# Performance work log

Hardware: AMD Instinct MI355X
Metric: run time of the kernel (lower is better)

Reference implementation:

```python
import jax, jax.numpy as jnp
import numpy as np

EMBED_DIM = 584  # module-global, used as softmax scale base (C ** -0.5)


def setup_inputs() -> dict:
    key = jax.random.key(0)
    ks = jax.random.split(key, 7)
    B, T, C, H, D = 16, 1024, 584, 8, 73
    x = jax.random.normal(ks[0], (B, T, C), dtype=jnp.float32)
    memory = jax.random.normal(ks[1], (B, T, C), dtype=jnp.float32)
    s = 0.02
    Wq = jax.random.normal(ks[2], (H, C, D), dtype=jnp.float32) * s
    Wk = jax.random.normal(ks[3], (H, C, D), dtype=jnp.float32) * s
    Wv = jax.random.normal(ks[4], (H, C, D), dtype=jnp.float32) * s
    Wp = jax.random.normal(ks[5], (C, C), dtype=jnp.float32) * s
    bp = jnp.zeros((C,), dtype=jnp.float32)
    return {"x": x, "memory": memory, "Wq": Wq, "Wk": Wk, "Wv": Wv, "Wp": Wp, "bp": bp}


def reference(x, memory, Wq, Wk, Wv, Wp, bp):
    B, T, C = x.shape
    # per-head projections, vectorized over heads: [B, H, T, D]
    q = jnp.einsum('btc,hcd->bhtd', x, Wq)
    k = jnp.einsum('bsc,hcd->bhsd', memory, Wk)
    v = jnp.einsum('btc,hcd->bhtd', x, Wv)  # NOTE: value from x, per original code
    # scale uses full embed dim C (not head size), per original code
    scores = jnp.einsum('bhtd,bhsd->bhts', q, k) * (C ** -0.5)
    weights = jax.nn.softmax(scores, axis=-1)
    # dropout is identity in eval/reference mode
    out = jnp.einsum('bhts,bhsd->bhtd', weights, v)  # requires S == T (matches original)
    out = out.transpose(0, 2, 1, 3).reshape(B, T, C)  # concat heads on last dim
    out = out @ Wp + bp  # output projection (dropout identity)
    return out
```

## Files before the change

### kernel.cpp

```cpp
#include <hip/hip_runtime.h>
#include <hip/hip_bf16.h>

typedef unsigned short u16;
typedef __attribute__((ext_vector_type(4))) unsigned short u16x4;
typedef __attribute__((ext_vector_type(8))) unsigned short u16x8;
typedef __attribute__((ext_vector_type(8))) __bf16 bf16x8;
typedef __attribute__((ext_vector_type(4))) float f32x4;

#define BB 16
#define TSEQ 1024
#define CC 584
#define HH 8
#define DHD 73
#define NR (BB*TSEQ)
#define KPW 640
#define DP 96
#define HD (HH*DP)
#define NP3 768
#define PPITCH 88
#define CEXP 0.0596985934f

__device__ __forceinline__ u16 f2bf(float f) {
  __bf16 h = (__bf16)f;
  return __builtin_bit_cast(u16, h);
}
__device__ __forceinline__ bf16x8 as_bf(u16x8 v) { return __builtin_bit_cast(bf16x8, v); }

#define GLL16(g, l) __builtin_amdgcn_global_load_lds( \
    (const __attribute__((address_space(1))) void*)(g), \
    (__attribute__((address_space(3))) void*)(l), 16, 0, 0)

#define BARRIER() asm volatile("s_barrier" ::: "memory")
#define LGKM0()   asm volatile("s_waitcnt lgkmcnt(0)" ::: "memory")
#define VMW4()    asm volatile("s_waitcnt vmcnt(4)" ::: "memory")
#define VMW0()    asm volatile("s_waitcnt vmcnt(0)" ::: "memory")

#define PKA 10240
#define PKB 5760
#define PKC 1920
__global__ void pack_all_kernel(const float* __restrict__ x, const float* __restrict__ mem,
                                const float* __restrict__ Wq, const float* __restrict__ Wk,
                                const float* __restrict__ Wv, const float* __restrict__ Wp,
                                u16* __restrict__ xmb, u16* __restrict__ wt,
                                u16* __restrict__ wpt) {
  const int bidx = blockIdx.x;
  const int tid = threadIdx.x;
  if (bidx < PKA) {
    int idx = bidx * 256 + tid;
    int row = idx / (KPW / 8);
    int c8  = (idx % (KPW / 8)) * 8;
    u16x8 o = {0, 0, 0, 0, 0, 0, 0, 0};
    if (c8 < CC) {
      const float* src = (row < NR) ? &x[(size_t)row * CC + c8]
                                    : &mem[(size_t)(row - NR) * CC + c8];
      f32x4 a = *(const f32x4*)src;
      f32x4 b = *(const f32x4*)(src + 4);
#pragma unroll
      for (int t = 0; t < 4; t++) { o[t] = f2bf(a[t]); o[4 + t] = f2bf(b[t]); }
    }
    *(u16x8*)&xmb[(size_t)row * KPW + c8] = o;
  } else if (bidx < PKA + PKB) {
    int idx = (bidx - PKA) * 256 + tid;
    int w   = idx / (HD * KPW);
    int rem = idx % (HD * KPW);
    int n = rem / KPW;
    int k = rem % KPW;
    int h = n / DP, d = n % DP;
    u16 val = 0;
    if (d < DHD && k < CC) {
      const float* W = (w == 0) ? Wq : ((w == 1) ? Wv : Wk);
      val = f2bf(W[((size_t)h * CC + k) * DHD + d]);
    }
    wt[idx] = val;
  } else {
    int idx = (bidx - PKA - PKB) * 256 + tid;
    int n = idx / KPW;
    int c = idx % KPW;
    u16 val = 0;
    if (n < CC && c < CC) val = f2bf(Wp[(size_t)c * CC + n]);
    wpt[idx] = val;
  }
}


template <int B, int MH>
__device__ __forceinline__ void lda_f(bf16x8 (&av)[4][2], const u16* lds,
                                      int aRow, int sw0, int sw1) {
#pragma unroll
  for (int mq = 0; mq < 4; mq++) {
    const int r = aRow + B * 16384 + MH * 4096 + mq * 1024;
    av[mq][0] = as_bf(*(const u16x8*)&lds[r + sw0]);
    av[mq][1] = as_bf(*(const u16x8*)&lds[r + sw1]);
  }
}
template <int B, int NH>
__device__ __forceinline__ void ldb_f(bf16x8 (&bv)[2][2], const u16* lds,
                                      int bRow, int sw0, int sw1) {
#pragma unroll
  for (int nq = 0; nq < 2; nq++) {
    const int r = 32768 + bRow + B * 16384 + NH * 2048 + nq * 1024;
    bv[nq][0] = as_bf(*(const u16x8*)&lds[r + sw0]);
    bv[nq][1] = as_bf(*(const u16x8*)&lds[r + sw1]);
  }
}
template <int OP, int U>
__device__ __forceinline__ void stg_f(const u16* g0, u16* l0, int t) {
  GLL16(g0 + (size_t)(U * 64) * KPW + (size_t)t * 64,
        l0 + OP * 32768 + (t & 1) * 16384 + U * 4096);
}
template <int MH, int NH>
__device__ __forceinline__ void mm_f(f32x4 (&acc)[8][4], const bf16x8 (&av)[4][2],
                                     const bf16x8 (&bv)[2][2]) {
  __builtin_amdgcn_s_setprio(1);
#pragma unroll
  for (int mq = 0; mq < 4; mq++)
#pragma unroll
    for (int nq = 0; nq < 2; nq++) {
      f32x4 c = acc[MH * 4 + mq][NH * 2 + nq];
      c = __builtin_amdgcn_mfma_f32_16x16x32_bf16(av[mq][0], bv[nq][0], c, 0, 0, 0);
      c = __builtin_amdgcn_mfma_f32_16x16x32_bf16(av[mq][1], bv[nq][1], c, 0, 0, 0);
      acc[MH * 4 + mq][NH * 2 + nq] = c;
    }
  __builtin_amdgcn_s_setprio(0);
}

template <int MODE>
__global__ __launch_bounds__(512, 2) void gemm8_kernel(
    const u16* __restrict__ A, const u16* __restrict__ Bt,
    void* __restrict__ CoutV, void* __restrict__ CoutV2,
    const float* __restrict__ bias) {
  extern __shared__ u16 lds[];
  const int tid  = threadIdx.x;
  const int lane = tid & 63;
  const int q15  = lane & 15;
  const int quad = lane >> 4;
  const int wave = tid >> 6;
  const int wmi  = wave >> 2;
  const int wni  = wave & 3;

  const int cpx = gridDim.x >> 3;
  const int bid = (blockIdx.x & 7) * cpx + (blockIdx.x >> 3);

  int m0, n0, npart;
  if (MODE == 4) {
    if (bid < 384) {
      m0 = (bid / 6) * 256; int nt = bid % 6;
      n0 = nt * 256; npart = (nt >= 3) ? 1 : 0;
    } else {
      int b2 = bid - 384;
      m0 = NR + (b2 / 3) * 256; n0 = 1536 + (b2 % 3) * 256; npart = 2;
    }
  } else {
    m0 = (bid / 3) * 256; n0 = (bid % 3) * 256; npart = 0;
  }

  const int tr   = tid >> 3;
  const int scol = ((tid & 7) ^ (tr & 7)) * 8;
  const u16* gA = &A[(size_t)(m0 + tr) * KPW + scol];
  const u16* gB = &Bt[(size_t)(n0 + tr) * KPW + scol];
  u16* ldst = &lds[tid * 8];

  const int rb  = q15 & 7;
  const int sw0 = (quad ^ rb) * 8;
  const int sw1 = ((quad + 4) ^ rb) * 8;
  const int aRow = (wmi * 128 + q15) * 64;
  const int bRow = (wni * 64 + q15) * 64;

  f32x4 acc[8][4];
#pragma unroll
  for (int i = 0; i < 8; i++)
#pragma unroll
    for (int j = 0; j < 4; j++) acc[i][j] = (f32x4){0.f, 0.f, 0.f, 0.f};
  bf16x8 av[4][2], bv[2][2];

  stg_f<0,0>(gA, ldst, 0); stg_f<0,1>(gA, ldst, 0);
  stg_f<0,2>(gA, ldst, 0); stg_f<0,3>(gA, ldst, 0);
  stg_f<1,0>(gB, ldst, 0); stg_f<1,1>(gB, ldst, 0);
  stg_f<1,2>(gB, ldst, 0); stg_f<1,3>(gB, ldst, 0);
  stg_f<0,0>(gA, ldst, 1); stg_f<0,2>(gA, ldst, 1);
  stg_f<0,1>(gA, ldst, 1); stg_f<0,3>(gA, ldst, 1);
  VMW4(); BARRIER();

#pragma unroll 1
  for (int i = 0; i < 5; ++i) {
    const int t1 = 2 * i + 1;
    const int t2 = 2 * i + 2;
    const bool st = (i < 4);
    lda_f<0,0>(av, lds, aRow, sw0, sw1);
    ldb_f<0,0>(bv, lds, bRow, sw0, sw1);
    stg_f<1,0>(gB, ldst, t1); stg_f<1,1>(gB, ldst, t1);
    stg_f<1,2>(gB, ldst, t1); stg_f<1,3>(gB, ldst, t1);
    BARRIER(); LGKM0();
    mm_f<0,0>(acc, av, bv);
    BARRIER();
    ldb_f<0,1>(bv, lds, bRow, sw0, sw1);
    if (st) { stg_f<0,0>(gA, ldst, t2); stg_f<0,2>(gA, ldst, t2); }
    BARRIER(); LGKM0();
    mm_f<0,1>(acc, av, bv);
    BARRIER();
    lda_f<0,1>(av, lds, aRow, sw0, sw1);
    ldb_f<0,0>(bv, lds, bRow, sw0, sw1);
    BARRIER(); LGKM0();
    mm_f<1,0>(acc, av, bv);
    BARRIER();
    ldb_f<0,1>(bv, lds, bRow, sw0, sw1);
    if (st) { stg_f<0,1>(gA, ldst, t2); stg_f<0,3>(gA, ldst, t2); }
    BARRIER(); LGKM0();
    mm_f<1,1>(acc, av, bv);
    if (st) { VMW4(); } else { VMW0(); }
    BARRIER();
    lda_f<1,0>(av, lds, aRow, sw0, sw1);
    ldb_f<1,0>(bv, lds, bRow, sw0, sw1);
    if (st) { stg_f<1,0>(gB, ldst, t2); stg_f<1,1>(gB, ldst, t2); }
    BARRIER(); LGKM0();
    mm_f<0,0>(acc, av, bv);
    BARRIER();
    ldb_f<1,1>(bv, lds, bRow, sw0, sw1);
    if (st) { stg_f<1,2>(gB, ldst, t2); stg_f<1,3>(gB, ldst, t2); }
    BARRIER(); LGKM0();
    mm_f<0,1>(acc, av, bv);
    BARRIER();
    lda_f<1,1>(av, lds, aRow, sw0, sw1);
    ldb_f<1,0>(bv, lds, bRow, sw0, sw1);
    if (st) { stg_f<0,0>(gA, ldst, t1 + 2); stg_f<0,2>(gA, ldst, t1 + 2); }
    BARRIER(); LGKM0();
    mm_f<1,0>(acc, av, bv);
    BARRIER();
    ldb_f<1,1>(bv, lds, bRow, sw0, sw1);
    if (st) { stg_f<0,1>(gA, ldst, t1 + 2); stg_f<0,3>(gA, ldst, t1 + 2); }
    BARRIER(); LGKM0();
    mm_f<1,1>(acc, av, bv);
    if (st) { VMW4(); }
    BARRIER();
  }

  const int rowb = m0 + wmi * 128 + quad * 4;
  const int colb = n0 + wni * 64 + q15;
  if (MODE == 4) {
    if (npart == 2) {
      u16* Cout = (u16*)CoutV2;
#pragma unroll
      for (int mf = 0; mf < 8; mf++)
#pragma unroll
        for (int nf = 0; nf < 4; nf++) {
          const int rk = rowb + mf * 16 - NR;
          const int ck = colb + nf * 16 - 1536;
#pragma unroll
          for (int r = 0; r < 4; r++)
            Cout[(size_t)(rk + r) * HD + ck] = f2bf(acc[mf][nf][r]);
        }
    } else if (npart == 0) {
      u16* Cout = (u16*)CoutV;
#pragma unroll
      for (int mf = 0; mf < 8; mf++)
#pragma unroll
        for (int nf = 0; nf < 4; nf++) {
          const int row = rowb + mf * 16;
          const int col = colb + nf * 16;
#pragma unroll
          for (int r = 0; r < 4; r++)
            Cout[(size_t)(row + r) * HD + col] = f2bf(acc[mf][nf][r]);
        }
    } else {
      u16* Cout = (u16*)CoutV;
#pragma unroll
      for (int mf = 0; mf < 8; mf++) {
        const int row = rowb + mf * 16;
        const int bb  = row >> 10;
        const int tl  = row & 1023;
#pragma unroll
        for (int nf = 0; nf < 4; nf++) {
          const int vn = colb + nf * 16 - HD;
          u16x4 pk;
#pragma unroll
          for (int r = 0; r < 4; r++) pk[r] = f2bf(acc[mf][nf][r]);
          *(u16x4*)&Cout[(size_t)(NR * HD) + ((size_t)(bb * HD + vn)) * TSEQ + tl] = pk;
        }
      }
    }
  } else {
    float* Cout = (float*)CoutV;
#pragma unroll
    for (int mf = 0; mf < 8; mf++)
#pragma unroll
      for (int nf = 0; nf < 4; nf++) {
        const int col = colb + nf * 16;
        if (col < CC) {
          const float bvv = bias[col];
          const int row = rowb + mf * 16;
#pragma unroll
          for (int r = 0; r < 4; r++)
            Cout[(size_t)(row + r) * CC + col] = acc[mf][nf][r] + bvv;
        }
      }
  }
}

__global__ __launch_bounds__(256, 3) void attn_kernel(
    const u16* __restrict__ qb, const u16* __restrict__ kb,
    const u16* __restrict__ vt, u16* __restrict__ attn) {
  __shared__ u16 smem[128 * 96 + 64 * 104 + 96 * 72];
  u16* Qs = smem;
  u16* Ks = smem + 128 * 96;
  u16* Vs = smem + 128 * 96 + 64 * 104;
  u16* Pt = smem;

  const int tid  = threadIdx.x;
  const int lane = tid & 63;
  const int wave = tid >> 6;
  const int q15  = lane & 15;
  const int quad = lane >> 4;
  const int bid  = blockIdx.x;
  const int loc  = bid >> 3;
  const int pair = (bid & 7) * 16 + (loc >> 3);
  const int b  = pair >> 3;
  const int h  = pair & 7;
  const int t0 = (loc & 7) * 128;
  const int wq0 = wave * 32;

  int krow[3], kc[3], vrow[3], vc[3];
#pragma unroll
  for (int p = 0; p < 3; p++) {
    int qk = tid + 256 * p;
    krow[p] = qk / 12; kc[p] = (qk % 12) * 8;
    int qv = tid + 256 * p;
    vrow[p] = qv / 8;  vc[p] = (qv % 8) * 8;
  }
  const u16* kbase = &kb[(size_t)(b * TSEQ) * HD + h * DP];
  const u16* vbase = &vt[(size_t)(b * HD + h * DP) * TSEQ];

  for (int q = tid; q < 128 * 12; q += 256) {
    int row = q / 12, c8 = (q % 12) * 8;
    *(u16x8*)&Qs[row * 96 + c8] =
        *(const u16x8*)&qb[(size_t)(b * TSEQ + t0 + row) * HD + h * DP + c8];
  }
  if (tid < 128) {
    const u16x8 z = {0, 0, 0, 0, 0, 0, 0, 0};
    size_t base = (size_t)(b * TSEQ + t0 + tid) * KPW + CC;
#pragma unroll
    for (int c = 0; c < (KPW - CC) / 8; c++) *(u16x8*)&attn[base + c * 8] = z;
  }
  __syncthreads();

  bf16x8 aq[2][3];
#pragma unroll
  for (int n = 0; n < 2; n++)
#pragma unroll
    for (int kcx = 0; kcx < 3; kcx++)
      aq[n][kcx] = as_bf(*(const u16x8*)&Qs[(wq0 + n * 16 + q15) * 96 + kcx * 32 + quad * 8]);

  float lsum[2] = {0.f, 0.f};
  f32x4 oacc[2][6];
#pragma unroll
  for (int m = 0; m < 2; m++)
#pragma unroll
    for (int jd = 0; jd < 6; jd++) oacc[m][jd] = (f32x4){0.f, 0.f, 0.f, 0.f};

  u16* Ptw = &Pt[wave * 32 * PPITCH];

  u16x8 kreg[3], vreg[3];
#pragma unroll
  for (int p = 0; p < 3; p++) {
    kreg[p] = *(const u16x8*)&kbase[(size_t)krow[p] * HD + kc[p]];
    vreg[p] = *(const u16x8*)&vbase[(size_t)vrow[p] * TSEQ + vc[p]];
  }

  for (int si = 0; si < 16; ++si) {
#pragma unroll
    for (int p = 0; p < 3; p++) {
      *(u16x8*)&Ks[krow[p] * 104 + kc[p]] = kreg[p];
      *(u16x8*)&Vs[vrow[p] * 72 + vc[p]]  = vreg[p];
    }
    __syncthreads();

    if (si < 15) {
      const int s1 = (si + 1) * 64;
#pragma unroll
      for (int p = 0; p < 3; p++) {
        kreg[p] = *(const u16x8*)&kbase[(size_t)(s1 + krow[p]) * HD + kc[p]];
        vreg[p] = *(const u16x8*)&vbase[(size_t)vrow[p] * TSEQ + s1 + vc[p]];
      }
    }

    f32x4 st[4][2];
#pragma unroll
    for (int mt = 0; mt < 4; mt++)
#pragma unroll
      for (int n = 0; n < 2; n++) st[mt][n] = (f32x4){0.f, 0.f, 0.f, 0.f};
#pragma unroll
    for (int kcx = 0; kcx < 3; kcx++) {
      bf16x8 ak[4];
#pragma unroll
      for (int mt = 0; mt < 4; mt++)
        ak[mt] = as_bf(*(const u16x8*)&Ks[(mt * 16 + q15) * 104 + kcx * 32 + quad * 8]);
#pragma unroll
      for (int mt = 0; mt < 4; mt++)
#pragma unroll
        for (int n = 0; n < 2; n++)
          st[mt][n] = __builtin_amdgcn_mfma_f32_16x16x32_bf16(ak[mt], aq[n][kcx], st[mt][n], 0, 0, 0);
    }

#pragma unroll
    for (int mt = 0; mt < 4; mt++)
#pragma unroll
      for (int n = 0; n < 2; n++) {
        f32x4 pv;
#pragma unroll
        for (int r = 0; r < 4; r++) pv[r] = __builtin_amdgcn_exp2f(st[mt][n][r] * CEXP);
        lsum[n] += (pv[0] + pv[1]) + (pv[2] + pv[3]);
        u16x4 pk;
#pragma unroll
        for (int r = 0; r < 4; r++) pk[r] = f2bf(pv[r]);
        *(u16x4*)&Ptw[(n * 16 + q15) * PPITCH + mt * 16 + quad * 4] = pk;
      }

#pragma unroll
    for (int kcx = 0; kcx < 2; kcx++) {
      bf16x8 ap[2];
#pragma unroll
      for (int m = 0; m < 2; m++)
        ap[m] = as_bf(*(const u16x8*)&Ptw[(m * 16 + q15) * PPITCH + kcx * 32 + quad * 8]);
#pragma unroll
      for (int jd = 0; jd < 6; jd++) {
        bf16x8 bv = as_bf(*(const u16x8*)&Vs[(jd * 16 + q15) * 72 + kcx * 32 + quad * 8]);
#pragma unroll
        for (int m = 0; m < 2; m++)
          oacc[m][jd] = __builtin_amdgcn_mfma_f32_16x16x32_bf16(ap[m], bv, oacc[m][jd], 0, 0, 0);
      }
    }
    __syncthreads();
  }

  float lr[2];
#pragma unroll
  for (int n = 0; n < 2; n++) {
    float s = lsum[n];
    s += __shfl_xor(s, 16);
    s += __shfl_xor(s, 32);
    lr[n] = s;
  }

#pragma unroll
  for (int m = 0; m < 2; m++) {
#pragma unroll
    for (int r = 0; r < 4; r++) {
      const float inv = 1.f / __shfl(lr[m], quad * 4 + r);
      const int trow = t0 + wq0 + m * 16 + quad * 4 + r;
#pragma unroll
      for (int jd = 0; jd < 5; jd++) {
        const int d = jd * 16 + q15;
        if (d < DHD)
          attn[(size_t)(b * TSEQ + trow) * KPW + h * DHD + d] = f2bf(oacc[m][jd][r] * inv);
      }
    }
  }
}


extern "C" void kernel_launch(void* const* d_in, const int* in_sizes, int n_in,
                              void* d_out, int out_size, void* d_ws, size_t ws_size,
                              hipStream_t stream) {
  const float* x   = (const float*)d_in[0];
  const float* mem = (const float*)d_in[1];
  const float* Wq  = (const float*)d_in[2];
  const float* Wk  = (const float*)d_in[3];
  const float* Wv  = (const float*)d_in[4];
  const float* Wp  = (const float*)d_in[5];
  const float* bp  = (const float*)d_in[6];
  float* out = (float*)d_out;

  char* ws = (char*)d_ws;
  const size_t SZ_XMB = (size_t)2 * NR * KPW * 2;
  const size_t SZ_WT  = (size_t)3 * HD * KPW * 2;
  const size_t SZ_WPT = (size_t)NP3 * KPW * 2;
  const size_t SZ_QB  = (size_t)NR * HD * 2;

  u16* xmb    = (u16*)(ws);
  u16* attn_o = (u16*)(ws);
  u16* wt     = (u16*)(ws + SZ_XMB);
  u16* wp_t   = (u16*)(ws + SZ_XMB + SZ_WT);
  u16* q_buf  = (u16*)(ws + SZ_XMB + SZ_WT + SZ_WPT);
  u16* vt_buf = q_buf + (size_t)NR * HD;
  u16* k_buf  = (u16*)(ws + SZ_XMB + SZ_WT + SZ_WPT + 2 * SZ_QB);

  (void)in_sizes; (void)n_in; (void)out_size; (void)ws_size;

  static bool s_attr = false;
  if (!s_attr) {
    (void)hipFuncSetAttribute((const void*)gemm8_kernel<4>,
                              hipFuncAttributeMaxDynamicSharedMemorySize, 131072);
    (void)hipFuncSetAttribute((const void*)gemm8_kernel<2>,
                              hipFuncAttributeMaxDynamicSharedMemorySize, 131072);
    s_attr = true;
  }

  pack_all_kernel<<<PKA + PKB + PKC, 256, 0, stream>>>(x, mem, Wq, Wk, Wv, Wp,
                                                       xmb, wt, wp_t);

  gemm8_kernel<4><<<576, 512, 131072, stream>>>(xmb, wt, q_buf, k_buf, nullptr);

  attn_kernel<<<BB * HH * (TSEQ / 128), 256, 0, stream>>>(q_buf, k_buf, vt_buf, attn_o);

  gemm8_kernel<2><<<192, 512, 131072, stream>>>(attn_o, wp_t, out, nullptr, bp);
}
```

Before: 292.2 us.

## Replace fine-grained 8-phase GEMM schedule with simple per-tile double-buffered loop

Replaces the hand-interleaved schedule, which had many barriers and half-tile LDS reads and global-to-LDS stages per iteration, with a plain loop. Each iteration loads the whole 64-wide K tile of A and B fragments from LDS, issues all MFMAs, then prefetches tile t+2 into the freed buffer, with two barriers per tile. This removes most barrier and lgkm wait overhead and lets the compiler schedule LDS reads against MFMAs. In exchange it uses more fragment registers and overlaps global loads with compute less finely.

```diff
diff --git a/kernel.cpp b/kernel.cpp
--- a/kernel.cpp
+++ b/kernel.cpp
@@ -14,6 +14,7 @@
 #define DHD 73
 #define NR (BB*TSEQ)
 #define KPW 640
+#define KT64 10
 #define DP 96
 #define HD (HH*DP)
 #define NP3 768
@@ -31,8 +32,7 @@
     (__attribute__((address_space(3))) void*)(l), 16, 0, 0)
 
 #define BARRIER() asm volatile("s_barrier" ::: "memory")
-#define LGKM0()   asm volatile("s_waitcnt lgkmcnt(0)" ::: "memory")
-#define VMW4()    asm volatile("s_waitcnt vmcnt(4)" ::: "memory")
+#define VMW8()    asm volatile("s_waitcnt vmcnt(8)" ::: "memory")
 #define VMW0()    asm volatile("s_waitcnt vmcnt(0)" ::: "memory")
 
 #define PKA 10240
@@ -83,31 +83,6 @@
 }
 
 
-template <int B, int MH>
-__device__ __forceinline__ void lda_f(bf16x8 (&av)[4][2], const u16* lds,
-                                      int aRow, int sw0, int sw1) {
-#pragma unroll
-  for (int mq = 0; mq < 4; mq++) {
-    const int r = aRow + B * 16384 + MH * 4096 + mq * 1024;
-    av[mq][0] = as_bf(*(const u16x8*)&lds[r + sw0]);
-    av[mq][1] = as_bf(*(const u16x8*)&lds[r + sw1]);
-  }
-}
-template <int B, int NH>
-__device__ __forceinline__ void ldb_f(bf16x8 (&bv)[2][2], const u16* lds,
-                                      int bRow, int sw0, int sw1) {
-#pragma unroll
-  for (int nq = 0; nq < 2; nq++) {
-    const int r = 32768 + bRow + B * 16384 + NH * 2048 + nq * 1024;
-    bv[nq][0] = as_bf(*(const u16x8*)&lds[r + sw0]);
-    bv[nq][1] = as_bf(*(const u16x8*)&lds[r + sw1]);
-  }
-}
-template <int OP, int U>
-__device__ __forceinline__ void stg_f(const u16* g0, u16* l0, int t) {
-  GLL16(g0 + (size_t)(U * 64) * KPW + (size_t)t * 64,
-        l0 + OP * 32768 + (t & 1) * 16384 + U * 4096);
-}
 template <int MH, int NH>
 __device__ __forceinline__ void mm_f(f32x4 (&acc)[8][4], const bf16x8 (&av)[4][2],
                                      const bf16x8 (&bv)[2][2]) {
@@ -122,6 +97,53 @@
       acc[MH * 4 + mq][NH * 2 + nq] = c;
     }
   __builtin_amdgcn_s_setprio(0);
+}
+
+__device__ __forceinline__ void compute_tile(f32x4 (&acc)[8][4], const u16* lds,
+                                             int bufA, int aRow, int bRow,
+                                             int sw0, int sw1) {
+  const int bufB = bufA + 32768;
+  bf16x8 a0[4][2], a1[4][2], b0[2][2], b1[2][2];
+#pragma unroll
+  for (int mq = 0; mq < 4; mq++) {
+    const int r = bufA + aRow + mq * 1024;
+    a0[mq][0] = as_bf(*(const u16x8*)&lds[r + sw0]);
+    a0[mq][1] = as_bf(*(const u16x8*)&lds[r + sw1]);
+  }
+#pragma unroll
+  for (int nq = 0; nq < 2; nq++) {
+    const int r = bufB + bRow + nq * 1024;
+    b0[nq][0] = as_bf(*(const u16x8*)&lds[r + sw0]);
+    b0[nq][1] = as_bf(*(const u16x8*)&lds[r + sw1]);
+  }
+#pragma unroll
+  for (int nq = 0; nq < 2; nq++) {
+    const int r = bufB + bRow + 2048 + nq * 1024;
+    b1[nq][0] = as_bf(*(const u16x8*)&lds[r + sw0]);
+    b1[nq][1] = as_bf(*(const u16x8*)&lds[r + sw1]);
+  }
+#pragma unroll
+  for (int mq = 0; mq < 4; mq++) {
+    const int r = bufA + aRow + 4096 + mq * 1024;
+    a1[mq][0] = as_bf(*(const u16x8*)&lds[r + sw0]);
+    a1[mq][1] = as_bf(*(const u16x8*)&lds[r + sw1]);
+  }
+  mm_f<0, 0>(acc, a0, b0);
+  mm_f<0, 1>(acc, a0, b1);
+  mm_f<1, 1>(acc, a1, b1);
+  mm_f<1, 0>(acc, a1, b0);
+}
+
+__device__ __forceinline__ void stage_all(const u16* gA, const u16* gB,
+                                          u16* ldst, int t) {
+  const size_t ko = (size_t)t * 64;
+  const int lb = (t & 1) * 16384;
+#pragma unroll
+  for (int U = 0; U < 4; U++)
+    GLL16(gA + (size_t)(U * 64) * KPW + ko, ldst + lb + U * 4096);
+#pragma unroll
+  for (int U = 0; U < 4; U++)
+    GLL16(gB + (size_t)(U * 64) * KPW + ko, ldst + 32768 + lb + U * 4096);
 }
 
 template <int MODE>
@@ -171,66 +193,22 @@
   for (int i = 0; i < 8; i++)
 #pragma unroll
     for (int j = 0; j < 4; j++) acc[i][j] = (f32x4){0.f, 0.f, 0.f, 0.f};
-  bf16x8 av[4][2], bv[2][2];
-
-  stg_f<0,0>(gA, ldst, 0); stg_f<0,1>(gA, ldst, 0);
-  stg_f<0,2>(gA, ldst, 0); stg_f<0,3>(gA, ldst, 0);
-  stg_f<1,0>(gB, ldst, 0); stg_f<1,1>(gB, ldst, 0);
-  stg_f<1,2>(gB, ldst, 0); stg_f<1,3>(gB, ldst, 0);
-  stg_f<0,0>(gA, ldst, 1); stg_f<0,2>(gA, ldst, 1);
-  stg_f<0,1>(gA, ldst, 1); stg_f<0,3>(gA, ldst, 1);
-  VMW4(); BARRIER();
+
+  stage_all(gA, gB, ldst, 0);
+  stage_all(gA, gB, ldst, 1);
+  VMW8(); BARRIER();
 
 #pragma unroll 1
-  for (int i = 0; i < 5; ++i) {
-    const int t1 = 2 * i + 1;
-    const int t2 = 2 * i + 2;
-    const bool st = (i < 4);
-    lda_f<0,0>(av, lds, aRow, sw0, sw1);
-    ldb_f<0,0>(bv, lds, bRow, sw0, sw1);
-    stg_f<1,0>(gB, ldst, t1); stg_f<1,1>(gB, ldst, t1);
-    stg_f<1,2>(gB, ldst, t1); stg_f<1,3>(gB, ldst, t1);
-    BARRIER(); LGKM0();
-    mm_f<0,0>(acc, av, bv);
+  for (int t = 0; t < KT64; ++t) {
+    compute_tile(acc, lds, (t & 1) * 16384, aRow, bRow, sw0, sw1);
+    if (t == KT64 - 1) break;
     BARRIER();
-    ldb_f<0,1>(bv, lds, bRow, sw0, sw1);
-    if (st) { stg_f<0,0>(gA, ldst, t2); stg_f<0,2>(gA, ldst, t2); }
-    BARRIER(); LGKM0();
-    mm_f<0,1>(acc, av, bv);
-    BARRIER();
-    lda_f<0,1>(av, lds, aRow, sw0, sw1);
-    ldb_f<0,0>(bv, lds, bRow, sw0, sw1);
-    BARRIER(); LGKM0();
-    mm_f<1,0>(acc, av, bv);
-    BARRIER();
-    ldb_f<0,1>(bv, lds, bRow, sw0, sw1);
-    if (st) { stg_f<0,1>(gA, ldst, t2); stg_f<0,3>(gA, ldst, t2); }
-    BARRIER(); LGKM0();
-    mm_f<1,1>(acc, av, bv);
-    if (st) { VMW4(); } else { VMW0(); }
-    BARRIER();
-    lda_f<1,0>(av, lds, aRow, sw0, sw1);
-    ldb_f<1,0>(bv, lds, bRow, sw0, sw1);
-    if (st) { stg_f<1,0>(gB, ldst, t2); stg_f<1,1>(gB, ldst, t2); }
-    BARRIER(); LGKM0();
-    mm_f<0,0>(acc, av, bv);
-    BARRIER();
-    ldb_f<1,1>(bv, lds, bRow, sw0, sw1);
-    if (st) { stg_f<1,2>(gB, ldst, t2); stg_f<1,3>(gB, ldst, t2); }
-    BARRIER(); LGKM0();
-    mm_f<0,1>(acc, av, bv);
-    BARRIER();
-    lda_f<1,1>(av, lds, aRow, sw0, sw1);
-    ldb_f<1,0>(bv, lds, bRow, sw0, sw1);
-    if (st) { stg_f<0,0>(gA, ldst, t1 + 2); stg_f<0,2>(gA, ldst, t1 + 2); }
-    BARRIER(); LGKM0();
-    mm_f<1,0>(acc, av, bv);
-    BARRIER();
-    ldb_f<1,1>(bv, lds, bRow, sw0, sw1);
-    if (st) { stg_f<0,1>(gA, ldst, t1 + 2); stg_f<0,3>(gA, ldst, t1 + 2); }
-    BARRIER(); LGKM0();
-    mm_f<1,1>(acc, av, bv);
-    if (st) { VMW4(); }
+    if (t + 2 < KT64) {
+      stage_all(gA, gB, ldst, t + 2);
+      VMW8();
+    } else {
+      VMW0();
+    }
     BARRIER();
   }
 
```

Result: no change. 295.6 us (+1.2%).

## Restructure GEMM into quadrant tiles with two B fragment registers and reordered staging

Applied to the files above, without the earlier changes.

Reorganizes the 256x256 GEMM tile so each wave owns four quadrants strided by 128 rows/cols. The LDS buffer layout changes to per-k-step buffers holding 128-row halves, and both B fragments are kept in registers (b0/b1) so A quadrants reuse B without rereading LDS. Global-to-LDS staging is regrouped into 128-row chunks with a different wait schedule. This aims to cut redundant LDS reads and smooth overlap between loads and MFMA, but it adds register pressure and changes the wait-count logic, which could stall or misorder loads.

```diff
diff --git a/kernel.cpp b/kernel.cpp
--- a/kernel.cpp
+++ b/kernel.cpp
@@ -33,6 +33,7 @@
 #define BARRIER() asm volatile("s_barrier" ::: "memory")
 #define LGKM0()   asm volatile("s_waitcnt lgkmcnt(0)" ::: "memory")
 #define VMW4()    asm volatile("s_waitcnt vmcnt(4)" ::: "memory")
+#define VMW2()    asm volatile("s_waitcnt vmcnt(2)" ::: "memory")
 #define VMW0()    asm volatile("s_waitcnt vmcnt(0)" ::: "memory")
 
 #define PKA 10240
@@ -83,42 +84,45 @@
 }
 
 
-template <int B, int MH>
-__device__ __forceinline__ void lda_f(bf16x8 (&av)[4][2], const u16* lds,
-                                      int aRow, int sw0, int sw1) {
+template <int BUF, int MH>
+__device__ __forceinline__ void rd_a(bf16x8 (&a)[4][2], const u16* lds, int arow,
+                                     int sw0, int sw1) {
 #pragma unroll
   for (int mq = 0; mq < 4; mq++) {
-    const int r = aRow + B * 16384 + MH * 4096 + mq * 1024;
-    av[mq][0] = as_bf(*(const u16x8*)&lds[r + sw0]);
-    av[mq][1] = as_bf(*(const u16x8*)&lds[r + sw1]);
-  }
-}
-template <int B, int NH>
-__device__ __forceinline__ void ldb_f(bf16x8 (&bv)[2][2], const u16* lds,
-                                      int bRow, int sw0, int sw1) {
+    const int r = BUF * 32768 + MH * 8192 + arow + mq * 1024;
+    a[mq][0] = as_bf(*(const u16x8*)&lds[r + sw0]);
+    a[mq][1] = as_bf(*(const u16x8*)&lds[r + sw1]);
+  }
+}
+template <int BUF, int NH>
+__device__ __forceinline__ void rd_b(bf16x8 (&b)[2][2], const u16* lds, int brow,
+                                     int sw0, int sw1) {
 #pragma unroll
   for (int nq = 0; nq < 2; nq++) {
-    const int r = 32768 + bRow + B * 16384 + NH * 2048 + nq * 1024;
-    bv[nq][0] = as_bf(*(const u16x8*)&lds[r + sw0]);
-    bv[nq][1] = as_bf(*(const u16x8*)&lds[r + sw1]);
-  }
-}
-template <int OP, int U>
-__device__ __forceinline__ void stg_f(const u16* g0, u16* l0, int t) {
-  GLL16(g0 + (size_t)(U * 64) * KPW + (size_t)t * 64,
-        l0 + OP * 32768 + (t & 1) * 16384 + U * 4096);
+    const int r = BUF * 32768 + 16384 + NH * 8192 + brow + nq * 1024;
+    b[nq][0] = as_bf(*(const u16x8*)&lds[r + sw0]);
+    b[nq][1] = as_bf(*(const u16x8*)&lds[r + sw1]);
+  }
+}
+template <int BUF, int RG>
+__device__ __forceinline__ void stg(const u16* gA, const u16* gB, u16* ldst, int t) {
+  const u16* src = (RG < 2) ? gA : gB;
+  const int rrow = (RG & 1) * 128;
+  const int loff = BUF * 32768 + (RG >> 1) * 16384 + (RG & 1) * 8192;
+  GLL16(src + (size_t)rrow * KPW + (size_t)t * 64, ldst + loff);
+  GLL16(src + (size_t)(rrow + 64) * KPW + (size_t)t * 64, ldst + loff + 4096);
 }
 template <int MH, int NH>
-__device__ __forceinline__ void mm_f(f32x4 (&acc)[8][4], const bf16x8 (&av)[4][2],
-                                     const bf16x8 (&bv)[2][2]) {
+__device__ __forceinline__ void mmq(f32x4 (&acc)[8][4], const bf16x8 (&a)[4][2],
+                                    const bf16x8 (&b)[2][2]) {
   __builtin_amdgcn_s_setprio(1);
 #pragma unroll
   for (int mq = 0; mq < 4; mq++)
 #pragma unroll
     for (int nq = 0; nq < 2; nq++) {
       f32x4 c = acc[MH * 4 + mq][NH * 2 + nq];
-      c = __builtin_amdgcn_mfma_f32_16x16x32_bf16(av[mq][0], bv[nq][0], c, 0, 0, 0);
-      c = __builtin_amdgcn_mfma_f32_16x16x32_bf16(av[mq][1], bv[nq][1], c, 0, 0, 0);
+      c = __builtin_amdgcn_mfma_f32_16x16x32_bf16(a[mq][0], b[nq][0], c, 0, 0, 0);
+      c = __builtin_amdgcn_mfma_f32_16x16x32_bf16(a[mq][1], b[nq][1], c, 0, 0, 0);
       acc[MH * 4 + mq][NH * 2 + nq] = c;
     }
   __builtin_amdgcn_s_setprio(0);
@@ -163,22 +167,20 @@
   const int rb  = q15 & 7;
   const int sw0 = (quad ^ rb) * 8;
   const int sw1 = ((quad + 4) ^ rb) * 8;
-  const int aRow = (wmi * 128 + q15) * 64;
-  const int bRow = (wni * 64 + q15) * 64;
+  const int arow = (wmi * 64 + q15) * 64;
+  const int brow = (wni * 32 + q15) * 64;
 
   f32x4 acc[8][4];
 #pragma unroll
   for (int i = 0; i < 8; i++)
 #pragma unroll
     for (int j = 0; j < 4; j++) acc[i][j] = (f32x4){0.f, 0.f, 0.f, 0.f};
-  bf16x8 av[4][2], bv[2][2];
-
-  stg_f<0,0>(gA, ldst, 0); stg_f<0,1>(gA, ldst, 0);
-  stg_f<0,2>(gA, ldst, 0); stg_f<0,3>(gA, ldst, 0);
-  stg_f<1,0>(gB, ldst, 0); stg_f<1,1>(gB, ldst, 0);
-  stg_f<1,2>(gB, ldst, 0); stg_f<1,3>(gB, ldst, 0);
-  stg_f<0,0>(gA, ldst, 1); stg_f<0,2>(gA, ldst, 1);
-  stg_f<0,1>(gA, ldst, 1); stg_f<0,3>(gA, ldst, 1);
+  bf16x8 a[4][2], b0[2][2], b1[2][2];
+
+  stg<0, 0>(gA, gB, ldst, 0);
+  stg<0, 2>(gA, gB, ldst, 0);
+  stg<0, 3>(gA, gB, ldst, 0);
+  stg<0, 1>(gA, gB, ldst, 0);
   VMW4(); BARRIER();
 
 #pragma unroll 1
@@ -186,114 +188,94 @@
     const int t1 = 2 * i + 1;
     const int t2 = 2 * i + 2;
     const bool st = (i < 4);
-    lda_f<0,0>(av, lds, aRow, sw0, sw1);
-    ldb_f<0,0>(bv, lds, bRow, sw0, sw1);
-    stg_f<1,0>(gB, ldst, t1); stg_f<1,1>(gB, ldst, t1);
-    stg_f<1,2>(gB, ldst, t1); stg_f<1,3>(gB, ldst, t1);
+    rd_a<0, 0>(a, lds, arow, sw0, sw1);
+    rd_b<0, 0>(b0, lds, brow, sw0, sw1);
+    stg<1, 0>(gA, gB, ldst, t1);
+    VMW4(); BARRIER(); LGKM0();
+    mmq<0, 0>(acc, a, b0);
+    BARRIER();
+    rd_b<0, 1>(b1, lds, brow, sw0, sw1);
+    stg<1, 2>(gA, gB, ldst, t1);
+    VMW4(); BARRIER(); LGKM0();
+    mmq<0, 1>(acc, a, b1);
+    BARRIER();
+    rd_a<0, 1>(a, lds, arow, sw0, sw1);
+    stg<1, 3>(gA, gB, ldst, t1);
+    VMW4(); BARRIER(); LGKM0();
+    mmq<1, 0>(acc, a, b0);
+    BARRIER();
+    stg<1, 1>(gA, gB, ldst, t1);
+    VMW4(); BARRIER();
+    mmq<1, 1>(acc, a, b1);
+    BARRIER();
+    rd_a<1, 0>(a, lds, arow, sw0, sw1);
+    rd_b<1, 0>(b0, lds, brow, sw0, sw1);
+    if (st) { stg<0, 0>(gA, gB, ldst, t2); VMW4(); } else { VMW2(); }
     BARRIER(); LGKM0();
-    mm_f<0,0>(acc, av, bv);
-    BARRIER();
-    ldb_f<0,1>(bv, lds, bRow, sw0, sw1);
-    if (st) { stg_f<0,0>(gA, ldst, t2); stg_f<0,2>(gA, ldst, t2); }
+    mmq<0, 0>(acc, a, b0);
+    BARRIER();
+    rd_b<1, 1>(b1, lds, brow, sw0, sw1);
+    if (st) { stg<0, 2>(gA, gB, ldst, t2); VMW4(); } else { VMW0(); }
     BARRIER(); LGKM0();
-    mm_f<0,1>(acc, av, bv);
-    BARRIER();
-    lda_f<0,1>(av, lds, aRow, sw0, sw1);
-    ldb_f<0,0>(bv, lds, bRow, sw0, sw1);
+    mmq<0, 1>(acc, a, b1);
+    BARRIER();
+    rd_a<1, 1>(a, lds, arow, sw0, sw1);
+    if (st) { stg<0, 3>(gA, gB, ldst, t2); VMW4(); }
     BARRIER(); LGKM0();
-    mm_f<1,0>(acc, av, bv);
-    BARRIER();
-    ldb_f<0,1>(bv, lds, bRow, sw0, sw1);
-    if (st) { stg_f<0,1>(gA, ldst, t2); stg_f<0,3>(gA, ldst, t2); }
-    BARRIER(); LGKM0();
-    mm_f<1,1>(acc, av, bv);
-    if (st) { VMW4(); } else { VMW0(); }
-    BARRIER();
-    lda_f<1,0>(av, lds, aRow, sw0, sw1);
-    ldb_f<1,0>(bv, lds, bRow, sw0, sw1);
-    if (st) { stg_f<1,0>(gB, ldst, t2); stg_f<1,1>(gB, ldst, t2); }
-    BARRIER(); LGKM0();
-    mm_f<0,0>(acc, av, bv);
-    BARRIER();
-    ldb_f<1,1>(bv, lds, bRow, sw0, sw1);
-    if (st) { stg_f<1,2>(gB, ldst, t2); stg_f<1,3>(gB, ldst, t2); }
-    BARRIER(); LGKM0();
-    mm_f<0,1>(acc, av, bv);
-    BARRIER();
-    lda_f<1,1>(av, lds, aRow, sw0, sw1);
-    ldb_f<1,0>(bv, lds, bRow, sw0, sw1);
-    if (st) { stg_f<0,0>(gA, ldst, t1 + 2); stg_f<0,2>(gA, ldst, t1 + 2); }
-    BARRIER(); LGKM0();
-    mm_f<1,0>(acc, av, bv);
-    BARRIER();
-    ldb_f<1,1>(bv, lds, bRow, sw0, sw1);
-    if (st) { stg_f<0,1>(gA, ldst, t1 + 2); stg_f<0,3>(gA, ldst, t1 + 2); }
-    BARRIER(); LGKM0();
-    mm_f<1,1>(acc, av, bv);
-    if (st) { VMW4(); }
-    BARRIER();
-  }
-
-  const int rowb = m0 + wmi * 128 + quad * 4;
-  const int colb = n0 + wni * 64 + q15;
-  if (MODE == 4) {
-    if (npart == 2) {
-      u16* Cout = (u16*)CoutV2;
-#pragma unroll
-      for (int mf = 0; mf < 8; mf++)
-#pragma unroll
-        for (int nf = 0; nf < 4; nf++) {
-          const int rk = rowb + mf * 16 - NR;
-          const int ck = colb + nf * 16 - 1536;
-#pragma unroll
-          for (int r = 0; r < 4; r++)
-            Cout[(size_t)(rk + r) * HD + ck] = f2bf(acc[mf][nf][r]);
+    mmq<1, 0>(acc, a, b0);
+    BARRIER();
+    if (st) { stg<0, 1>(gA, gB, ldst, t2); VMW4(); }
+    BARRIER();
+    mmq<1, 1>(acc, a, b1);
+    BARRIER();
+  }
+
+  const int rowb = m0 + wmi * 64 + quad * 4;
+  const int colb = n0 + wni * 32 + q15;
+#pragma unroll
+  for (int mh = 0; mh < 2; mh++)
+#pragma unroll
+    for (int mq = 0; mq < 4; mq++)
+#pragma unroll
+      for (int nh = 0; nh < 2; nh++)
+#pragma unroll
+        for (int nq = 0; nq < 2; nq++) {
+          const f32x4 av = acc[mh * 4 + mq][nh * 2 + nq];
+          const int row = rowb + mh * 128 + mq * 16;
+          const int col = colb + nh * 128 + nq * 16;
+          if (MODE == 4) {
+            if (npart == 2) {
+              u16* Cout = (u16*)CoutV2;
+              const int rk = row - NR;
+              const int ck = col - 1536;
+#pragma unroll
+              for (int r = 0; r < 4; r++)
+                Cout[(size_t)(rk + r) * HD + ck] = f2bf(av[r]);
+            } else if (npart == 0) {
+              u16* Cout = (u16*)CoutV;
+#pragma unroll
+              for (int r = 0; r < 4; r++)
+                Cout[(size_t)(row + r) * HD + col] = f2bf(av[r]);
+            } else {
+              u16* Cout = (u16*)CoutV;
+              const int vn = col - HD;
+              const int bb = row >> 10;
+              const int tl = row & 1023;
+              u16x4 pk;
+#pragma unroll
+              for (int r = 0; r < 4; r++) pk[r] = f2bf(av[r]);
+              *(u16x4*)&Cout[(size_t)(NR * HD) + ((size_t)(bb * HD + vn)) * TSEQ + tl] = pk;
+            }
+          } else {
+            if (col < CC) {
+              float* Cout = (float*)CoutV;
+              const float bvv = bias[col];
+#pragma unroll
+              for (int r = 0; r < 4; r++)
+                Cout[(size_t)(row + r) * CC + col] = av[r] + bvv;
+            }
+          }
         }
-    } else if (npart == 0) {
-      u16* Cout = (u16*)CoutV;
-#pragma unroll
-      for (int mf = 0; mf < 8; mf++)
-#pragma unroll
-        for (int nf = 0; nf < 4; nf++) {
-          const int row = rowb + mf * 16;
-          const int col = colb + nf * 16;
-#pragma unroll
-          for (int r = 0; r < 4; r++)
-            Cout[(size_t)(row + r) * HD + col] = f2bf(acc[mf][nf][r]);
-        }
-    } else {
-      u16* Cout = (u16*)CoutV;
-#pragma unroll
-      for (int mf = 0; mf < 8; mf++) {
-        const int row = rowb + mf * 16;
-        const int bb  = row >> 10;
-        const int tl  = row & 1023;
-#pragma unroll
-        for (int nf = 0; nf < 4; nf++) {
-          const int vn = colb + nf * 16 - HD;
-          u16x4 pk;
-#pragma unroll
-          for (int r = 0; r < 4; r++) pk[r] = f2bf(acc[mf][nf][r]);
-          *(u16x4*)&Cout[(size_t)(NR * HD) + ((size_t)(bb * HD + vn)) * TSEQ + tl] = pk;
-        }
-      }
-    }
-  } else {
-    float* Cout = (float*)CoutV;
-#pragma unroll
-    for (int mf = 0; mf < 8; mf++)
-#pragma unroll
-      for (int nf = 0; nf < 4; nf++) {
-        const int col = colb + nf * 16;
-        if (col < CC) {
-          const float bvv = bias[col];
-          const int row = rowb + mf * 16;
-#pragma unroll
-          for (int r = 0; r < 4; r++)
-            Cout[(size_t)(row + r) * CC + col] = acc[mf][nf][r] + bvv;
-        }
-      }
-  }
 }
 
 __global__ __launch_bounds__(256, 3) void attn_kernel(
```

Result: no change. 291.8 us (-0.2%).
